# Performance work log

Hardware: AMD Instinct MI355X
Metric: run time of the kernel (lower is better)

## Reference

```python
import jax, jax.numpy as jnp
import numpy as np

B, L, D, H, NL, F, C = 32, 512, 512, 8, 6, 2048, 9
HD = D // H
SCALE = float(np.sqrt(HD))
EPS = 1e-5


def _layernorm(x, g, b):
    mu = jnp.mean(x, axis=-1, keepdims=True)
    var = jnp.mean((x - mu) ** 2, axis=-1, keepdims=True)
    return (x - mu) * jax.lax.rsqrt(var + EPS) * g + b


def setup_inputs() -> dict:
    key = jax.random.key(0)
    ks = jax.random.split(key, 16)
    s = 0.02
    return {
        "x": jax.random.normal(ks[0], (B, L, D), jnp.float32),
        "case_ids": jax.random.randint(ks[1], (B, L), 0, C),
        "attention_mask": jnp.ones((B, L), jnp.int32),
        "Wq": jax.random.normal(ks[2], (NL, D, D), jnp.float32) * s,
        "bq": jnp.zeros((NL, D), jnp.float32),
        "Wk": jax.random.normal(ks[3], (NL, D, D), jnp.float32) * s,
        "bk": jnp.zeros((NL, D), jnp.float32),
        "Wv": jax.random.normal(ks[4], (NL, D, D), jnp.float32) * s,
        "bv": jnp.zeros((NL, D), jnp.float32),
        "Wo": jax.random.normal(ks[5], (NL, D, D), jnp.float32) * s,
        "bo": jnp.zeros((NL, D), jnp.float32),
        "ln1_g": jnp.ones((NL, D), jnp.float32),
        "ln1_b": jnp.zeros((NL, D), jnp.float32),
        "ln2_g": jnp.ones((NL, D), jnp.float32),
        "ln2_b": jnp.zeros((NL, D), jnp.float32),
        "W1": jax.random.normal(ks[6], (NL, D, F), jnp.float32) * s,
        "b1": jnp.zeros((NL, F), jnp.float32),
        "W2": jax.random.normal(ks[7], (NL, F, D), jnp.float32) * s,
        "b2": jnp.zeros((NL, D), jnp.float32),
        "case_bias": jax.random.normal(ks[8], (NL, H, C, C), jnp.float32) * 0.1,
        "verb_bias": jax.random.normal(ks[9], (NL, H), jnp.float32) * 0.1,
        "fn_g": jnp.ones((D,), jnp.float32),
        "fn_b": jnp.zeros((D,), jnp.float32),
    }


def reference(x, case_ids, attention_mask, Wq, bq, Wk, bk, Wv, bv, Wo, bo,
              ln1_g, ln1_b, ln2_g, ln2_b, W1, b1, W2, b2,
              case_bias, verb_bias, fn_g, fn_b):
    dt = x.dtype
    # causal + padding additive mask: [B, 1, L, L]
    causal = jnp.triu(jnp.full((L, L), -10000.0, dtype=dt), k=1)[None, None]
    pad = (1.0 - attention_mask.astype(dt))[:, None, None, :] * -10000.0
    mask = causal + pad
    verb_mask = (case_ids == 8).astype(dt)  # [B, L]
    ci, cj = case_ids[:, :, None], case_ids[:, None, :]  # [B,L,1], [B,1,L]

    for i in range(NL):
        h = _layernorm(x, ln1_g[i], ln1_b[i])
        q = (h @ Wq[i] + bq[i]).reshape(B, L, H, HD).transpose(0, 2, 1, 3)
        k = (h @ Wk[i] + bk[i]).reshape(B, L, H, HD).transpose(0, 2, 1, 3)
        v = (h @ Wv[i] + bv[i]).reshape(B, L, H, HD).transpose(0, 2, 1, 3)
        scores = jnp.einsum('bhqd,bhkd->bhqk', q, k) / SCALE
        # Panini grammatical bias: per-head pairwise case bias + verb key bias
        pbias = case_bias[i][:, ci, cj]  # [H, B, L, L]
        scores = scores + jnp.transpose(pbias, (1, 0, 2, 3))
        scores = scores + verb_bias[i][None, :, None, None] * verb_mask[:, None, None, :]
        scores = scores + mask
        w = jax.nn.softmax(scores, axis=-1)
        attn = jnp.einsum('bhqk,bhkd->bhqd', w, v).transpose(0, 2, 1, 3).reshape(B, L, D)
        x = x + attn @ Wo[i] + bo[i]
        h2 = _layernorm(x, ln2_g[i], ln2_b[i])
        ff = jax.nn.gelu(h2 @ W1[i] + b1[i], approximate=False) @ W2[i] + b2[i]
        x = x + ff
    return _layernorm(x, fn_g, fn_b)
```

## Files before the change

### kernel.cpp

```cpp
#include <hip/hip_runtime.h>
#include <hip/hip_bf16.h>

#define B_   32
#define L_   512
#define D_   512
#define H_   8
#define NL_  6
#define F_   2048
#define C_   9
#define HD_  64
#define MTOK 16384

typedef __bf16 bf16x8 __attribute__((ext_vector_type(8)));
typedef __bf16 bf16x4 __attribute__((ext_vector_type(4)));
typedef float  f32x4  __attribute__((ext_vector_type(4)));

#define MFMA16(a,b,c) __builtin_amdgcn_mfma_f32_16x16x32_bf16((a),(b),(c),0,0,0)
#define GLD16(g,l) __builtin_amdgcn_global_load_lds( \
    (const __attribute__((address_space(1))) void*)(g), \
    (__attribute__((address_space(3))) void*)(l), 16, 0, 0)

__global__ __launch_bounds__(256) void transpose_w(
    const float* __restrict__ in, __hip_bfloat16* __restrict__ out,
    int K, int N, size_t zso)
{
    __shared__ float t[32][33];
    const int z = blockIdx.z;
    const float* src = in + (size_t)z * K * N;
    __hip_bfloat16* dst = out + (size_t)z * zso;
    const int n0 = blockIdx.x * 32, k0 = blockIdx.y * 32;
    const int tx = threadIdx.x, ty = threadIdx.y;
#pragma unroll
    for (int r = ty; r < 32; r += 8)
        t[r][tx] = src[(size_t)(k0 + r) * N + n0 + tx];
    __syncthreads();
#pragma unroll
    for (int r = ty; r < 32; r += 8)
        dst[(size_t)(n0 + r) * K + k0 + tx] = __float2bfloat16(t[tx][r]);
}

__global__ void copy_f32x4(const float4* __restrict__ in, float4* __restrict__ out, int n)
{
    int i = blockIdx.x * blockDim.x + threadIdx.x;
    if (i < n) out[i] = in[i];
}

__global__ __launch_bounds__(256) void bias_build(
    const int* __restrict__ case_ids, const int* __restrict__ amask,
    const float* __restrict__ cbias, const float* __restrict__ vbias,
    __hip_bfloat16* __restrict__ tab)
{
    const unsigned idx = blockIdx.x * 256 + threadIdx.x;
    const int kv = idx & 511;
    unsigned r = idx >> 9;
    const int ci = r % 9; r /= 9;
    const int hh = r % H_; r /= H_;
    const int b = r % B_; const int l = r / B_;
    const int cj = case_ids[b * L_ + kv];
    const float v = cbias[(((size_t)l * H_ + hh) * C_ + ci) * C_ + cj]
                  + (cj == 8 ? vbias[l * H_ + hh] : 0.f)
                  - 10000.f * (1.f - (float)amask[b * L_ + kv]);
    tab[idx] = __float2bfloat16(v);
}

template <typename OUT>
__global__ __launch_bounds__(256) void ln_kernel(
    const float* __restrict__ x, const float* __restrict__ g,
    const float* __restrict__ be, OUT* __restrict__ out)
{
    const int row  = blockIdx.x * 4 + (threadIdx.x >> 6);
    const int lane = threadIdx.x & 63;
    const int c0   = lane * 8;
    const float* xr = x + (size_t)row * D_ + c0;
    float4 a = *(const float4*)xr;
    float4 c = *(const float4*)(xr + 4);
    float v[8] = {a.x, a.y, a.z, a.w, c.x, c.y, c.z, c.w};

    float s = 0.f;
#pragma unroll
    for (int j = 0; j < 8; ++j) s += v[j];
#pragma unroll
    for (int o = 1; o < 64; o <<= 1) s += __shfl_xor(s, o, 64);
    const float mu = s * (1.0f / D_);

    float s2 = 0.f;
#pragma unroll
    for (int j = 0; j < 8; ++j) { float d = v[j] - mu; s2 += d * d; }
#pragma unroll
    for (int o = 1; o < 64; o <<= 1) s2 += __shfl_xor(s2, o, 64);
    const float rs = rsqrtf(s2 * (1.0f / D_) + 1e-5f);

    float4 g0 = *(const float4*)(g + c0);
    float4 g1 = *(const float4*)(g + c0 + 4);
    float4 b0 = *(const float4*)(be + c0);
    float4 b1 = *(const float4*)(be + c0 + 4);
    float gg[8] = {g0.x, g0.y, g0.z, g0.w, g1.x, g1.y, g1.z, g1.w};
    float bb[8] = {b0.x, b0.y, b0.z, b0.w, b1.x, b1.y, b1.z, b1.w};

    if constexpr (sizeof(OUT) == 2) {
        bf16x8 o8;
#pragma unroll
        for (int j = 0; j < 8; ++j)
            o8[j] = (__bf16)((v[j] - mu) * rs * gg[j] + bb[j]);
        *(bf16x8*)((__hip_bfloat16*)out + (size_t)row * D_ + c0) = o8;
    } else {
        float* op = (float*)out + (size_t)row * D_ + c0;
        float4 r0, r1;
        r0.x = (v[0]-mu)*rs*gg[0]+bb[0]; r0.y = (v[1]-mu)*rs*gg[1]+bb[1];
        r0.z = (v[2]-mu)*rs*gg[2]+bb[2]; r0.w = (v[3]-mu)*rs*gg[3]+bb[3];
        r1.x = (v[4]-mu)*rs*gg[4]+bb[4]; r1.y = (v[5]-mu)*rs*gg[5]+bb[5];
        r1.z = (v[6]-mu)*rs*gg[6]+bb[6]; r1.w = (v[7]-mu)*rs*gg[7]+bb[7];
        *(float4*)op = r0; *(float4*)(op + 4) = r1;
    }
}

__device__ __forceinline__ float gelu_tanh(float v)
{
    const float t2 = v * v;
    const float u  = v * (0.7978845608028654f + 0.0356774081363001f * t2);
    const float a  = __builtin_fabsf(u);
    const float e  = __expf(-2.0f * a);
    const float r  = __builtin_amdgcn_rcpf(1.0f + e);
    const float th = (1.0f - e) * r;
    return 0.5f * v + 0.5f * __builtin_fabsf(v) * th;
}

template <int EPI, int WM>
__global__ __launch_bounds__(WM * 128, (WM == 4) ? 4 : 3) void gemm_r5(
    const __hip_bfloat16* __restrict__ A,
    const __hip_bfloat16* __restrict__ BT,
    const float* __restrict__ bias0, const float* __restrict__ bias1,
    const float* __restrict__ bias2,
    void* __restrict__ out0, void* __restrict__ out1, void* __restrict__ out2,
    const float* __restrict__ Res, int Ndim, int K)
{
    constexpr int THREADS = WM * 128;
    constexpr int BM = WM * 64;
    __shared__ __align__(16) __hip_bfloat16 As[3][BM * 32];
    __shared__ __align__(16) __hip_bfloat16 Bs[3][128 * 32];

    const int tid = threadIdx.x;
    const int w = tid >> 6, lane = tid & 63;
    const int lq = lane & 15, lg = lane >> 4;
    const int wm = w >> 1, wn = w & 1;
    const int RB = wm * 64, CB = wn * 64;

    const int gX = gridDim.x;
    const int nwg = gX * gridDim.y;
    int flat = blockIdx.y * gX + blockIdx.x;
    {
        const int qq = nwg >> 3, rr = nwg & 7;
        const int xcd = flat & 7, off = flat >> 3;
        flat = (xcd < rr ? xcd * (qq + 1) : rr * (qq + 1) + (xcd - rr) * qq) + off;
    }
    const int bx = flat % gX, by = flat / gX;
    const int m0 = by * BM, n0 = bx * 128;

    const int rc = tid >> 2;
    const int sc = ((tid & 3) ^ ((rc >> 1) & 3)) * 8;
    const __hip_bfloat16* gA0 = A  + (size_t)(m0 + rc) * K + sc;
    const __hip_bfloat16* gB0 = BT + (size_t)(n0 + rc) * K + sc;

    auto STAGE = [&](int tt) {
        const size_t ko = (size_t)tt * 32;
        const int sl = tt % 3;
        char* ab = (char*)As[sl] + w * 1024;
        GLD16(gA0 + ko, ab);
        GLD16(gA0 + (size_t)(THREADS / 4) * K + ko, ab + THREADS * 16);
        char* bb = (char*)Bs[sl] + w * 1024;
        GLD16(gB0 + ko, bb);
        if constexpr (WM == 2)
            GLD16(gB0 + (size_t)64 * K + ko, bb + 4096);
    };

    const int rsw = (lq >> 1) & 3;
    const int aoff = (RB + lq) * 64 + ((lg ^ rsw) << 4);
    const int boff = (CB + lq) * 64 + ((lg ^ rsw) << 4);

    f32x4 acc[4][4] = {};
    const int NTt = K >> 5;

    STAGE(0); STAGE(1);

    for (int t = 0; t < NTt; ++t) {
        if (t + 1 < NTt) {
            if constexpr (WM == 4) asm volatile("s_waitcnt vmcnt(3)" ::: "memory");
            else                   asm volatile("s_waitcnt vmcnt(4)" ::: "memory");
        } else {
            asm volatile("s_waitcnt vmcnt(0)" ::: "memory");
        }
        __builtin_amdgcn_s_barrier();
        __builtin_amdgcn_sched_barrier(0);

        const char* ca = (const char*)As[t % 3];
        const char* cb = (const char*)Bs[t % 3];
        bf16x8 af[4], bf[4];
#pragma unroll
        for (int fm = 0; fm < 4; ++fm) af[fm] = *(const bf16x8*)(ca + aoff + fm * 1024);
#pragma unroll
        for (int fn = 0; fn < 4; ++fn) bf[fn] = *(const bf16x8*)(cb + boff + fn * 1024);

        if (t + 2 < NTt) STAGE(t + 2);

        __builtin_amdgcn_s_setprio(1);
#pragma unroll
        for (int fm = 0; fm < 4; ++fm)
#pragma unroll
            for (int fn = 0; fn < 4; ++fn)
                acc[fm][fn] = MFMA16(af[fm], bf[fn], acc[fm][fn]);
        __builtin_amdgcn_s_setprio(0);
    }

    if constexpr (EPI == 4) {
        const int sec = n0 >> 9;
        const int nb = (n0 & 511) + CB;
        const float* bp = sec == 0 ? bias0 : (sec == 1 ? bias1 : bias2);
        float bcol[4];
#pragma unroll
        for (int fn = 0; fn < 4; ++fn) bcol[fn] = bp[nb + fn * 16 + lq];
        if (sec < 2) {
            __hip_bfloat16* op = (__hip_bfloat16*)(sec == 0 ? out0 : out1);
#pragma unroll
            for (int fm = 0; fm < 4; ++fm)
#pragma unroll
                for (int fn = 0; fn < 4; ++fn)
#pragma unroll
                    for (int r = 0; r < 4; ++r) {
                        const int m = m0 + RB + fm * 16 + lg * 4 + r;
                        op[(size_t)m * 512 + nb + fn * 16 + lq] =
                            __float2bfloat16(acc[fm][fn][r] + bcol[fn]);
                    }
        } else {
            __hip_bfloat16* vp = (__hip_bfloat16*)out2;
            const int bb = m0 >> 9;
            const int l0 = (m0 & 511) + RB + lg * 4;
#pragma unroll
            for (int fm = 0; fm < 4; ++fm)
#pragma unroll
                for (int fn = 0; fn < 4; ++fn) {
                    bf16x4 pv;
#pragma unroll
                    for (int r = 0; r < 4; ++r)
                        pv[r] = (__bf16)(acc[fm][fn][r] + bcol[fn]);
                    *(bf16x4*)(vp + ((size_t)(bb * 512 + nb + fn * 16 + lq)) * 512
                               + l0 + fm * 16) = pv;
                }
        }
    } else {
        float bcol[4];
#pragma unroll
        for (int fn = 0; fn < 4; ++fn) bcol[fn] = bias0[n0 + CB + fn * 16 + lq];
#pragma unroll
        for (int fm = 0; fm < 4; ++fm)
#pragma unroll
            for (int fn = 0; fn < 4; ++fn) {
                const int n = n0 + CB + fn * 16 + lq;
#pragma unroll
                for (int r = 0; r < 4; ++r) {
                    const int m = m0 + RB + fm * 16 + lg * 4 + r;
                    float v = acc[fm][fn][r] + bcol[fn];
                    if constexpr (EPI == 1) {
                        float* Co = (float*)out0;
                        const size_t idx = (size_t)m * Ndim + n;
                        Co[idx] = Res[idx] + v;
                    } else {
                        ((__hip_bfloat16*)out0)[(size_t)m * Ndim + n] =
                            __float2bfloat16(gelu_tanh(v));
                    }
                }
            }
    }
}

__global__ __launch_bounds__(256, 4) void attn_kernel(
    const __hip_bfloat16* __restrict__ Q, const __hip_bfloat16* __restrict__ K,
    const __hip_bfloat16* __restrict__ VT, __hip_bfloat16* __restrict__ Out,
    const int* __restrict__ case_ids, const __hip_bfloat16* __restrict__ tab,
    int layer)
{
    __shared__ __align__(16) __bf16 Ks[2][64 * 64];
    __shared__ __align__(16) __bf16 Vs[2][64 * 64];
    __shared__ __align__(16) __bf16 Pl[4][16 * 64];

    const int bh = blockIdx.x;
    const int b = bh >> 3, hh = bh & 7;
    const int qcA = blockIdx.y;
    const int qcB = 7 - qcA;
    const int t = threadIdx.x;
    const int w = t >> 6, lane = t & 63;
    const int lq = lane & 15, lg = lane >> 4;
    const int swz = lq & 7;

    const int rA = w * 16 + (lane >> 3);
    const int swsrc = ((lane & 7) ^ (lane >> 3)) << 4;
    const __hip_bfloat16* kg0 = K  + ((size_t)b * L_ + rA) * D_ + hh * HD_;
    const __hip_bfloat16* vg0 = VT + ((size_t)b * D_ + hh * HD_ + rA) * L_;

    auto stage = [&](int buf, int kv0) {
        const char* gk = (const char*)(kg0 + (size_t)kv0 * D_) + swsrc;
        GLD16(gk,                      (char*)Ks[buf] + w * 2048);
        GLD16(gk + (size_t)8 * D_ * 2, (char*)Ks[buf] + w * 2048 + 1024);
        const char* gv = (const char*)(vg0 + kv0) + swsrc;
        GLD16(gv,                      (char*)Vs[buf] + w * 2048);
        GLD16(gv + (size_t)8 * L_ * 2, (char*)Vs[buf] + w * 2048 + 1024);
    };

    stage(0, 0);

    const int qloc = w * 16 + lq;
    const int qrowA = qcA * 64 + qloc;
    const int qrowB = qcB * 64 + qloc;
    const size_t tbase = (((size_t)layer * B_ + b) * H_ + hh) * C_;
    const __hip_bfloat16* ciqA = tab + (tbase + case_ids[b * L_ + qrowA]) * L_;
    const __hip_bfloat16* ciqB = tab + (tbase + case_ids[b * L_ + qrowB]) * L_;

    const __hip_bfloat16* qpA = Q + ((size_t)b * L_ + qrowA) * D_ + hh * HD_;
    const __hip_bfloat16* qpB = Q + ((size_t)b * L_ + qrowB) * D_ + hh * HD_;
    const bf16x8 qfA0 = *(const bf16x8*)(qpA + lg * 8);
    const bf16x8 qfA1 = *(const bf16x8*)(qpA + 32 + lg * 8);
    const bf16x8 qfB0 = *(const bf16x8*)(qpB + lg * 8);
    const bf16x8 qfB1 = *(const bf16x8*)(qpB + 32 + lg * 8);

    float mA = -1e30f, lA = 0.f, mB = -1e30f, lB = 0.f;
    f32x4 oA[4] = {}, oB[4] = {};
    int cur = 0;

    auto process = [&](const bf16x8 qf0, const bf16x8 qf1,
                       const __hip_bfloat16* ciq, int qcX,
                       float& m_run, float& l_run, f32x4* o,
                       const char* kb, const char* vb2, int kt) {
        bf16x4 bb[4];
#pragma unroll
        for (int c = 0; c < 4; ++c)
            bb[c] = *(const bf16x4*)(ciq + kt * 64 + 16 * c + lg * 4);

        f32x4 s[4] = {};
        __builtin_amdgcn_s_setprio(1);
#pragma unroll
        for (int c = 0; c < 4; ++c) {
            const bf16x8 ka = *(const bf16x8*)(kb + (16 * c + lq) * 128 + ((lg ^ swz) << 4));
            s[c] = MFMA16(ka, qf0, s[c]);
            const bf16x8 kc = *(const bf16x8*)(kb + (16 * c + lq) * 128 + (((4 + lg) ^ swz) << 4));
            s[c] = MFMA16(kc, qf1, s[c]);
        }
        __builtin_amdgcn_s_setprio(0);

        const bool dtile = (kt == qcX);
        float xs[16];
#pragma unroll
        for (int c = 0; c < 4; ++c)
#pragma unroll
            for (int r = 0; r < 4; ++r) {
                const int kvl = 16 * c + lg * 4 + r;
                float v = s[c][r] * 0.125f + (float)bb[c][r];
                xs[4 * c + r] = (dtile && (kvl > qloc)) ? -1e9f : v;
            }

        float a0 = fmaxf(fmaxf(xs[0], xs[1]),  fmaxf(xs[2], xs[3]));
        float a1 = fmaxf(fmaxf(xs[4], xs[5]),  fmaxf(xs[6], xs[7]));
        float a2 = fmaxf(fmaxf(xs[8], xs[9]),  fmaxf(xs[10], xs[11]));
        float a3 = fmaxf(fmaxf(xs[12], xs[13]), fmaxf(xs[14], xs[15]));
        float pmax = fmaxf(fmaxf(a0, a1), fmaxf(a2, a3));
        pmax = fmaxf(pmax, __shfl_xor(pmax, 16, 64));
        pmax = fmaxf(pmax, __shfl_xor(pmax, 32, 64));

        const float mnew = fmaxf(m_run, pmax);
        const float corr = __expf(m_run - mnew);
        float ps = 0.f;
#pragma unroll
        for (int j = 0; j < 16; ++j) { xs[j] = __expf(xs[j] - mnew); ps += xs[j]; }
        ps += __shfl_xor(ps, 16, 64);
        ps += __shfl_xor(ps, 32, 64);
        l_run = l_run * corr + ps;
        m_run = mnew;

        float cr[4];
#pragma unroll
        for (int r = 0; r < 4; ++r) cr[r] = __shfl(corr, lg * 4 + r, 64);
#pragma unroll
        for (int nt = 0; nt < 4; ++nt)
#pragma unroll
            for (int r = 0; r < 4; ++r) o[nt][r] *= cr[r];

        char* pw = (char*)Pl[w];
#pragma unroll
        for (int c = 0; c < 4; ++c) {
            bf16x4 pv;
#pragma unroll
            for (int r = 0; r < 4; ++r) pv[r] = (__bf16)xs[4 * c + r];
            const int slot = (2 * c + (lg >> 1)) ^ swz;
            *(bf16x4*)(pw + lq * 128 + (slot << 4) + ((lg & 1) << 3)) = pv;
        }

        __builtin_amdgcn_s_setprio(1);
#pragma unroll
        for (int hf = 0; hf < 2; ++hf) {
            const bf16x8 pf = *(const bf16x8*)(pw + lq * 128 + (((hf * 4 + lg) ^ swz) << 4));
#pragma unroll
            for (int nt = 0; nt < 4; ++nt) {
                const bf16x8 vf = *(const bf16x8*)(vb2 + (nt * 16 + lq) * 128
                                                   + (((hf * 4 + lg) ^ swz) << 4));
                o[nt] = MFMA16(pf, vf, o[nt]);
            }
        }
        __builtin_amdgcn_s_setprio(0);
    };

    for (int kt = 0; kt <= qcB; ++kt) {
        if (kt) __builtin_amdgcn_s_barrier();
        if (kt < qcB) {
            stage(cur ^ 1, (kt + 1) * 64);
            asm volatile("s_waitcnt vmcnt(4)" ::: "memory");
        } else {
            asm volatile("s_waitcnt vmcnt(0)" ::: "memory");
        }
        __builtin_amdgcn_s_barrier();
        __builtin_amdgcn_sched_barrier(0);

        const char* kb  = (const char*)Ks[cur];
        const char* vb2 = (const char*)Vs[cur];

        process(qfB0, qfB1, ciqB, qcB, mB, lB, oB, kb, vb2, kt);
        if (kt <= qcA)
            process(qfA0, qfA1, ciqA, qcA, mA, lA, oA, kb, vb2, kt);
        cur ^= 1;
    }

    auto writeout = [&](float l_run, f32x4* o, int qcX) {
        const float inv = 1.f / l_run;
        float ir[4];
#pragma unroll
        for (int r = 0; r < 4; ++r) ir[r] = __shfl(inv, lg * 4 + r, 64);
        __hip_bfloat16* op = Out + ((size_t)b * L_ + qcX * 64 + w * 16) * D_ + hh * HD_;
#pragma unroll
        for (int nt = 0; nt < 4; ++nt)
#pragma unroll
            for (int r = 0; r < 4; ++r)
                op[(size_t)(lg * 4 + r) * D_ + nt * 16 + lq] =
                    __float2bfloat16(o[nt][r] * ir[r]);
    };
    writeout(lA, oA, qcA);
    writeout(lB, oB, qcB);
}

extern "C" void kernel_launch(void* const* d_in, const int* in_sizes, int n_in,
                              void* d_out, int out_size, void* d_ws, size_t ws_size,
                              hipStream_t stream)
{
    const float* x_in  = (const float*)d_in[0];
    const int*   cids  = (const int*)  d_in[1];
    const int*   amask = (const int*)  d_in[2];
    const float* Wq = (const float*)d_in[3];
    const float* bq = (const float*)d_in[4];
    const float* Wk = (const float*)d_in[5];
    const float* bk = (const float*)d_in[6];
    const float* Wv = (const float*)d_in[7];
    const float* bv = (const float*)d_in[8];
    const float* Wo = (const float*)d_in[9];
    const float* bo = (const float*)d_in[10];
    const float* ln1g = (const float*)d_in[11];
    const float* ln1b = (const float*)d_in[12];
    const float* ln2g = (const float*)d_in[13];
    const float* ln2b = (const float*)d_in[14];
    const float* W1 = (const float*)d_in[15];
    const float* b1 = (const float*)d_in[16];
    const float* W2 = (const float*)d_in[17];
    const float* b2 = (const float*)d_in[18];
    const float* cbias = (const float*)d_in[19];
    const float* vbias = (const float*)d_in[20];
    const float* fng = (const float*)d_in[21];
    const float* fnb = (const float*)d_in[22];

    char* w = (char*)d_ws;
    float* x_ws = (float*)w;                 w += (size_t)MTOK * D_ * 4;
    __hip_bfloat16* hbuf = (__hip_bfloat16*)w; w += (size_t)MTOK * D_ * 2;
    __hip_bfloat16* qbuf = (__hip_bfloat16*)w; w += (size_t)MTOK * D_ * 2;
    __hip_bfloat16* kbuf = (__hip_bfloat16*)w; w += (size_t)MTOK * D_ * 2;
    __hip_bfloat16* vtb  = (__hip_bfloat16*)w; w += (size_t)MTOK * D_ * 2;
    __hip_bfloat16* ffb  = (__hip_bfloat16*)w; w += (size_t)MTOK * F_ * 2;
    __hip_bfloat16* WqkvT = (__hip_bfloat16*)w; w += (size_t)NL_ * 3 * D_ * D_ * 2;
    __hip_bfloat16* WoT  = (__hip_bfloat16*)w; w += (size_t)NL_ * D_ * D_ * 2;
    __hip_bfloat16* W1T  = (__hip_bfloat16*)w; w += (size_t)NL_ * D_ * F_ * 2;
    __hip_bfloat16* W2T  = (__hip_bfloat16*)w; w += (size_t)NL_ * D_ * F_ * 2;
    __hip_bfloat16* btab = (__hip_bfloat16*)w; w += (size_t)NL_ * B_ * H_ * C_ * L_ * 2;

    const size_t qkvZ = (size_t)3 * D_ * D_;
    const dim3 tb(32, 8);
    transpose_w<<<dim3(D_/32, D_/32, NL_), tb, 0, stream>>>(Wq, WqkvT,           D_, D_, qkvZ);
    transpose_w<<<dim3(D_/32, D_/32, NL_), tb, 0, stream>>>(Wk, WqkvT + D_*D_,   D_, D_, qkvZ);
    transpose_w<<<dim3(D_/32, D_/32, NL_), tb, 0, stream>>>(Wv, WqkvT + 2*D_*D_, D_, D_, qkvZ);
    transpose_w<<<dim3(D_/32, D_/32, NL_), tb, 0, stream>>>(Wo, WoT, D_, D_, (size_t)D_*D_);
    transpose_w<<<dim3(F_/32, D_/32, NL_), tb, 0, stream>>>(W1, W1T, D_, F_, (size_t)D_*F_);
    transpose_w<<<dim3(D_/32, F_/32, NL_), tb, 0, stream>>>(W2, W2T, F_, D_, (size_t)D_*F_);

    bias_build<<<(NL_ * B_ * H_ * C_ * L_) / 256, 256, 0, stream>>>(
        cids, amask, cbias, vbias, btab);

    copy_f32x4<<<8192, 256, 0, stream>>>((const float4*)x_in, (float4*)x_ws,
                                         MTOK * D_ / 4);

    const dim3 gQKV(12, 128);
    const dim3 gO(4, 128);
    const dim3 gW1(16, 64);
    const dim3 gW2(4, 128);

    for (int i = 0; i < NL_; ++i) {
        ln_kernel<__hip_bfloat16><<<MTOK/4, 256, 0, stream>>>(
            x_ws, ln1g + i * D_, ln1b + i * D_, hbuf);

        gemm_r5<4, 2><<<gQKV, 256, 0, stream>>>(hbuf, WqkvT + (size_t)i * qkvZ,
            bq + i*D_, bk + i*D_, bv + i*D_, qbuf, kbuf, vtb, nullptr, 512, D_);

        attn_kernel<<<dim3(B_ * H_, 4), 256, 0, stream>>>(
            qbuf, kbuf, vtb, hbuf, cids, btab, i);

        gemm_r5<1, 2><<<gO, 256, 0, stream>>>(hbuf, WoT + (size_t)i*D_*D_,
            bo + i*D_, nullptr, nullptr, x_ws, nullptr, nullptr, x_ws, D_, D_);

        ln_kernel<__hip_bfloat16><<<MTOK/4, 256, 0, stream>>>(
            x_ws, ln2g + i * D_, ln2b + i * D_, hbuf);

        gemm_r5<2, 4><<<gW1, 512, 0, stream>>>(hbuf, W1T + (size_t)i*D_*F_,
            b1 + i*F_, nullptr, nullptr, ffb, nullptr, nullptr, nullptr, F_, D_);

        gemm_r5<1, 2><<<gW2, 256, 0, stream>>>(ffb, W2T + (size_t)i*D_*F_,
            b2 + i*D_, nullptr, nullptr, x_ws, nullptr, nullptr, x_ws, D_, F_);
    }

    ln_kernel<float><<<MTOK/4, 256, 0, stream>>>(x_ws, fng, fnb, (float*)d_out);
}
```

Baseline: 1.277 ms.

## Add dedicated 256x256-tile W1 GEMM kernel with 4-stage LDS pipeline

Replaces the generic W1 up-projection GEMM with a specialised kernel that uses 256x256 output tiles, 8 waves in a 2x4 layout, a 4-deep direct-to-LDS prefetch ring, and remapping of workgroups across the XCDs. Each K step is split into two MFMA phases, with loads interleaved between them and waves given raised priority while they issue MFMAs. The goal is more data reuse per tile and better overlap of global loads with compute for the largest GEMM. In exchange the kernel uses 128 KB of LDS and many accumulator registers, which caps occupancy, and the grid of 512 blocks may not balance evenly across CUs.

```diff
diff --git a/kernel.cpp b/kernel.cpp
--- a/kernel.cpp
+++ b/kernel.cpp
@@ -270,6 +270,124 @@
                 }
             }
     }
+}
+
+__global__ __launch_bounds__(512, 2) void gemm_w1(
+    const __hip_bfloat16* __restrict__ A,
+    const __hip_bfloat16* __restrict__ BT,
+    const float* __restrict__ bias,
+    __hip_bfloat16* __restrict__ out, int Ndim, int K)
+{
+    __shared__ __align__(16) __hip_bfloat16 As[4][256 * 32];
+    __shared__ __align__(16) __hip_bfloat16 Bs[4][256 * 32];
+
+    const int tid = threadIdx.x;
+    const int w = tid >> 6, lane = tid & 63;
+    const int lq = lane & 15, lg = lane >> 4;
+    const int wm = w >> 2, wn = w & 3;
+    const int RB = wm * 128, CB = wn * 64;
+
+    const int gX = gridDim.x;
+    const int nwg = gX * gridDim.y;
+    int flat = blockIdx.y * gX + blockIdx.x;
+    {
+        const int qq = nwg >> 3, rr = nwg & 7;
+        const int xcd = flat & 7, off = flat >> 3;
+        flat = (xcd < rr ? xcd * (qq + 1) : rr * (qq + 1) + (xcd - rr) * qq) + off;
+    }
+    const int bx = flat % gX, by = flat / gX;
+    const int m0 = by * 256, n0 = bx * 256;
+
+    const int rc = tid >> 2;
+    const int sc = ((tid & 3) ^ ((rc >> 1) & 3)) * 8;
+    const __hip_bfloat16* gA0 = A  + (size_t)(m0 + rc) * K + sc;
+    const __hip_bfloat16* gB0 = BT + (size_t)(n0 + rc) * K + sc;
+
+    auto STAGE_A = [&](int tt) {
+        const size_t ko = (size_t)tt * 32;
+        char* ab = (char*)As[tt & 3] + w * 1024;
+        GLD16(gA0 + ko, ab);
+        GLD16(gA0 + (size_t)128 * K + ko, ab + 8192);
+    };
+    auto STAGE_B = [&](int tt) {
+        const size_t ko = (size_t)tt * 32;
+        char* bb = (char*)Bs[tt & 3] + w * 1024;
+        GLD16(gB0 + ko, bb);
+        GLD16(gB0 + (size_t)128 * K + ko, bb + 8192);
+    };
+
+    const int rsw = (lq >> 1) & 3;
+    const int aoff = (RB + lq) * 64 + ((lg ^ rsw) << 4);
+    const int boff = (CB + lq) * 64 + ((lg ^ rsw) << 4);
+
+    f32x4 acc[8][4] = {};
+    const int NTt = K >> 5;
+
+    STAGE_A(0); STAGE_B(0);
+    STAGE_A(1); STAGE_B(1);
+    STAGE_A(2); STAGE_B(2);
+    asm volatile("s_waitcnt vmcnt(8)" ::: "memory");
+    __builtin_amdgcn_s_barrier();
+
+    for (int t = 0; t < NTt; ++t) {
+        const char* ca = (const char*)As[t & 3];
+        const char* cb = (const char*)Bs[t & 3];
+
+        __builtin_amdgcn_sched_barrier(0);
+        bf16x8 af[4], bf[4];
+#pragma unroll
+        for (int fm = 0; fm < 4; ++fm) af[fm] = *(const bf16x8*)(ca + aoff + fm * 1024);
+#pragma unroll
+        for (int fn = 0; fn < 4; ++fn) bf[fn] = *(const bf16x8*)(cb + boff + fn * 1024);
+        if (t + 3 < NTt) STAGE_A(t + 3);
+        __builtin_amdgcn_s_barrier();
+        __builtin_amdgcn_sched_barrier(0);
+        __builtin_amdgcn_s_setprio(1);
+#pragma unroll
+        for (int fm = 0; fm < 4; ++fm)
+#pragma unroll
+            for (int fn = 0; fn < 4; ++fn)
+                acc[fm][fn] = MFMA16(af[fm], bf[fn], acc[fm][fn]);
+        __builtin_amdgcn_s_setprio(0);
+        __builtin_amdgcn_s_barrier();
+
+        __builtin_amdgcn_sched_barrier(0);
+        bf16x8 ag[4];
+#pragma unroll
+        for (int fm = 0; fm < 4; ++fm) ag[fm] = *(const bf16x8*)(ca + aoff + (fm + 4) * 1024);
+        if (t + 3 < NTt) STAGE_B(t + 3);
+        if (t + 1 < NTt) {
+            if (t + 3 < NTt)      asm volatile("s_waitcnt vmcnt(8)" ::: "memory");
+            else if (t + 2 < NTt) asm volatile("s_waitcnt vmcnt(4)" ::: "memory");
+            else                  asm volatile("s_waitcnt vmcnt(0)" ::: "memory");
+        }
+        __builtin_amdgcn_s_barrier();
+        __builtin_amdgcn_sched_barrier(0);
+        __builtin_amdgcn_s_setprio(1);
+#pragma unroll
+        for (int fm = 0; fm < 4; ++fm)
+#pragma unroll
+            for (int fn = 0; fn < 4; ++fn)
+                acc[fm + 4][fn] = MFMA16(ag[fm], bf[fn], acc[fm + 4][fn]);
+        __builtin_amdgcn_s_setprio(0);
+        __builtin_amdgcn_s_barrier();
+    }
+
+    float bcol[4];
+#pragma unroll
+    for (int fn = 0; fn < 4; ++fn) bcol[fn] = bias[n0 + CB + fn * 16 + lq];
+#pragma unroll
+    for (int fm = 0; fm < 8; ++fm)
+#pragma unroll
+        for (int fn = 0; fn < 4; ++fn) {
+            const int n = n0 + CB + fn * 16 + lq;
+#pragma unroll
+            for (int r = 0; r < 4; ++r) {
+                const int m = m0 + RB + fm * 16 + lg * 4 + r;
+                out[(size_t)m * Ndim + n] =
+                    __float2bfloat16(gelu_tanh(acc[fm][fn][r] + bcol[fn]));
+            }
+        }
 }
 
 __global__ __launch_bounds__(256, 4) void attn_kernel(
@@ -501,7 +619,7 @@
 
     const dim3 gQKV(12, 128);
     const dim3 gO(4, 128);
-    const dim3 gW1(16, 64);
+    const dim3 gW1(8, 64);
     const dim3 gW2(4, 128);
 
     for (int i = 0; i < NL_; ++i) {
@@ -520,8 +638,8 @@
         ln_kernel<__hip_bfloat16><<<MTOK/4, 256, 0, stream>>>(
             x_ws, ln2g + i * D_, ln2b + i * D_, hbuf);
 
-        gemm_r5<2, 4><<<gW1, 512, 0, stream>>>(hbuf, W1T + (size_t)i*D_*F_,
-            b1 + i*F_, nullptr, nullptr, ffb, nullptr, nullptr, nullptr, F_, D_);
+        gemm_w1<<<gW1, 512, 0, stream>>>(hbuf, W1T + (size_t)i*D_*F_,
+            b1 + i*F_, ffb, F_, D_);
 
         gemm_r5<1, 2><<<gW2, 256, 0, stream>>>(ffb, W2T + (size_t)i*D_*F_,
             b2 + i*D_, nullptr, nullptr, x_ws, nullptr, nullptr, x_ws, D_, F_);
```

Measured after the change: 1.280 ms. No clear change (+0.2%).
